# Optimization experiments

Measured on AMD Instinct MI355X. Metric: run time of the kernel, lower is better.

Reference implementation:

```python
import jax, jax.numpy as jnp
import numpy as np

N_NODES = 100000
N_EDGES = 1600000
NODE_DIM = 64
EDGE_DIM = 16
HIDDEN = 64
N_LAYERS = 3
N_GRAPHS = 512
BN_EPS = 1e-5


def setup_inputs() -> dict:
    key = jax.random.key(0)
    ks = jax.random.split(key, 12)
    x = jax.random.normal(ks[0], (N_NODES, NODE_DIM), dtype=jnp.float32)
    edge_index = jax.random.randint(ks[1], (2, N_EDGES), 0, N_NODES, dtype=jnp.int32)
    edge_attr = jax.random.normal(ks[2], (N_EDGES, EDGE_DIM), dtype=jnp.float32)
    batch = jnp.sort(jax.random.randint(ks[3], (N_NODES,), 0, N_GRAPHS, dtype=jnp.int32))
    s = 0.1
    # stacked per-layer params (node_dim == hidden so all layers share shapes)
    We = jax.random.normal(ks[4], (N_LAYERS, EDGE_DIM, HIDDEN), dtype=jnp.float32) * s
    be = jnp.zeros((N_LAYERS, HIDDEN), dtype=jnp.float32)
    W1 = jax.random.normal(ks[5], (N_LAYERS, HIDDEN, HIDDEN), dtype=jnp.float32) * s
    b1 = jnp.zeros((N_LAYERS, HIDDEN), dtype=jnp.float32)
    W2 = jax.random.normal(ks[6], (N_LAYERS, HIDDEN, HIDDEN), dtype=jnp.float32) * s
    b2 = jnp.zeros((N_LAYERS, HIDDEN), dtype=jnp.float32)
    gamma = jnp.ones((N_LAYERS, HIDDEN), dtype=jnp.float32)
    beta = jnp.zeros((N_LAYERS, HIDDEN), dtype=jnp.float32)
    return {"x": x, "edge_attr": edge_attr, "We": We, "be": be, "W1": W1,
            "b1": b1, "W2": W2, "b2": b2, "gamma": gamma, "beta": beta,
            "edge_index": edge_index, "batch": batch}


def reference(x, edge_attr, We, be, W1, b1, W2, b2, gamma, beta, edge_index, batch):
    src, dst = edge_index[0], edge_index[1]
    n_nodes = x.shape[0]
    z = x
    zs = []
    for l in range(We.shape[0]):
        # GINEConv: message = relu(x_j + Lin(edge_attr)); aggr = scatter_add at dst
        e = edge_attr @ We[l] + be[l]                       # [E, H]
        msg = jax.nn.relu(z[src] + e)                       # [E, H]
        aggr = jax.ops.segment_sum(msg, dst, num_segments=n_nodes)  # [N, H]
        h = z + aggr                                        # (1 + eps)*x, eps=0
        h = jax.nn.relu(h @ W1[l] + b1[l]) @ W2[l] + b2[l]  # GINE nn MLP
        h = jax.nn.relu(h)
        # BatchNorm1d in training mode: biased batch stats over nodes
        mean = jnp.mean(h, axis=0)
        var = jnp.mean(jnp.square(h - mean), axis=0)
        h = gamma[l] * (h - mean) * jax.lax.rsqrt(var + BN_EPS) + beta[l]
        z = h
        zs.append(h)
    zz = jnp.concatenate(zs, axis=1)                        # [N, L*H]
    g = jax.ops.segment_sum(zz, batch, num_segments=N_GRAPHS)  # [G, L*H]
    return zz, g
```

## Files before the change

kernel.cpp:

```cpp
#include <hip/hip_runtime.h>

#define N_NODES 100000
#define N_EDGES 1600000
#define HIDDEN 64
#define EDGE_DIM 16
#define N_LAYERS 3
#define N_GRAPHS 512
#define BN_EPS 1e-5f

#define CHUNK 2048
#define NCHUNK ((N_NODES + CHUNK - 1) / CHUNK)

typedef _Float16 h2 __attribute__((ext_vector_type(2)));
typedef _Float16 h4 __attribute__((ext_vector_type(4)));


__global__ void k_hist(const int* __restrict__ dst, int* __restrict__ hist) {
    int e = blockIdx.x * 256 + threadIdx.x;
    if (e < N_EDGES) atomicAdd(&hist[dst[e]], 1);
}

__global__ void k_scan_partial(const int* __restrict__ hist, int* __restrict__ partial) {
    __shared__ int sd[256];
    int c = blockIdx.x, t = threadIdx.x;
    int base = c * CHUNK + t * 8;
    int s = 0;
#pragma unroll
    for (int u = 0; u < 8; ++u) {
        int i = base + u;
        s += (i < N_NODES) ? hist[i] : 0;
    }
    sd[t] = s;
    __syncthreads();
    for (int d = 128; d > 0; d >>= 1) {
        if (t < d) sd[t] += sd[t + d];
        __syncthreads();
    }
    if (t == 0) partial[c] = sd[0];
}

__global__ void k_scan_base(const int* __restrict__ partial, int* __restrict__ cbase) {
    if (threadIdx.x == 0) {
        int r = 0;
        for (int c = 0; c < NCHUNK; ++c) { cbase[c] = r; r += partial[c]; }
    }
}

__global__ void k_scan_final(const int* __restrict__ hist, const int* __restrict__ cbase,
                             int* __restrict__ row_start, int* __restrict__ cursor) {
    __shared__ int sd[256];
    int c = blockIdx.x, t = threadIdx.x;
    int i0 = c * CHUNK + t * 8;
    int v[8];
    int s = 0;
#pragma unroll
    for (int u = 0; u < 8; ++u) {
        int i = i0 + u;
        v[u] = (i < N_NODES) ? hist[i] : 0;
        s += v[u];
    }
    sd[t] = s;
    __syncthreads();
    for (int d = 1; d < 256; d <<= 1) {
        int x = (t >= d) ? sd[t - d] : 0;
        __syncthreads();
        sd[t] += x;
        __syncthreads();
    }
    int run = cbase[c] + sd[t] - s;
#pragma unroll
    for (int u = 0; u < 8; ++u) {
        int i = i0 + u;
        if (i <= N_NODES) { row_start[i] = run; cursor[i] = run; }
        run += v[u];
    }
}

__global__ void k_fill_es(const int* __restrict__ edge_index, int* __restrict__ cursor,
                          int2* __restrict__ es_sorted) {
    int e = blockIdx.x * 256 + threadIdx.x;
    if (e >= N_EDGES) return;
    int s = edge_index[e];
    int d = edge_index[N_EDGES + e];
    int p = atomicAdd(&cursor[d], 1);
    es_sorted[p] = make_int2(e, s);
}

__global__ __launch_bounds__(256) void k_gather(const int2* __restrict__ es,
        const float* __restrict__ ea, _Float16* __restrict__ ea16,
        int* __restrict__ src_sorted) {
    int gid = blockIdx.x * 256 + threadIdx.x;
    if (gid >= N_EDGES * 4) return;
    int p = gid >> 2, part = gid & 3;
    int2 r = es[p];
    if (part == 0) src_sorted[p] = r.y;
    float4 v = ((const float4*)(ea + (size_t)r.x * 16))[part];
    h4 o = {(_Float16)v.x, (_Float16)v.y, (_Float16)v.z, (_Float16)v.w};
    ((h4*)(ea16 + (size_t)p * 16))[part] = o;
}

__global__ __launch_bounds__(256) void k_cvt_x(const float* __restrict__ x,
                                               _Float16* __restrict__ x16) {
    int i = blockIdx.x * 256 + threadIdx.x;
    if (i >= N_NODES * 16) return;
    float4 v = ((const float4*)x)[i];
    h4 o = {(_Float16)v.x, (_Float16)v.y, (_Float16)v.z, (_Float16)v.w};
    ((h4*)x16)[i] = o;
}


__global__ __launch_bounds__(256) void k_aggregate(
        const float* __restrict__ zself_base, int zstride,
        const _Float16* __restrict__ z16,
        const float* __restrict__ We, const float* __restrict__ be,
        const int* __restrict__ row_start,
        const int* __restrict__ srcs, const _Float16* __restrict__ ea16,
        float* __restrict__ hin) {
    int gid = blockIdx.x * 256 + threadIdx.x;
    int node = __builtin_amdgcn_readfirstlane(gid >> 6);
    int lane = threadIdx.x & 63;
    if (node >= N_NODES) return;
    h2 w2[8];
#pragma unroll
    for (int i = 0; i < 8; ++i) {
        h2 t;
        t[0] = (_Float16)We[(2 * i) * 64 + lane];
        t[1] = (_Float16)We[(2 * i + 1) * 64 + lane];
        w2[i] = t;
    }
    float bl = be[lane];
    int p0 = row_start[node], p1 = row_start[node + 1];
    float acc = 0.f;
    int p = p0;
    for (; p + 8 <= p1; p += 8) {
        int s[8];
        float zv[8], ev[8];
#pragma unroll
        for (int u = 0; u < 8; ++u) s[u] = srcs[p + u];
#pragma unroll
        for (int u = 0; u < 8; ++u) zv[u] = (float)z16[(size_t)s[u] * 64 + lane];
#pragma unroll
        for (int u = 0; u < 8; ++u) {
            const h2* row = (const h2*)(ea16 + (size_t)(p + u) * 16);
            float e = bl;
#pragma unroll
            for (int i = 0; i < 8; ++i) e = __builtin_amdgcn_fdot2(row[i], w2[i], e, false);
            ev[u] = e;
        }
#pragma unroll
        for (int u = 0; u < 8; ++u) acc += fmaxf(zv[u] + ev[u], 0.f);
    }
    for (; p + 4 <= p1; p += 4) {
        int s[4];
        float zv[4], ev[4];
#pragma unroll
        for (int u = 0; u < 4; ++u) s[u] = srcs[p + u];
#pragma unroll
        for (int u = 0; u < 4; ++u) zv[u] = (float)z16[(size_t)s[u] * 64 + lane];
#pragma unroll
        for (int u = 0; u < 4; ++u) {
            const h2* row = (const h2*)(ea16 + (size_t)(p + u) * 16);
            float e = bl;
#pragma unroll
            for (int i = 0; i < 8; ++i) e = __builtin_amdgcn_fdot2(row[i], w2[i], e, false);
            ev[u] = e;
        }
#pragma unroll
        for (int u = 0; u < 4; ++u) acc += fmaxf(zv[u] + ev[u], 0.f);
    }
    for (; p < p1; ++p) {
        int s = srcs[p];
        const h2* row = (const h2*)(ea16 + (size_t)p * 16);
        float zv = (float)z16[(size_t)s * 64 + lane];
        float e = bl;
#pragma unroll
        for (int i = 0; i < 8; ++i) e = __builtin_amdgcn_fdot2(row[i], w2[i], e, false);
        acc += fmaxf(zv + e, 0.f);
    }
    float zself = zself_base[(size_t)node * zstride + lane];
    hin[(size_t)node * 64 + lane] = zself + acc;
}

__global__ __launch_bounds__(256) void k_mlp(
        const float* __restrict__ hin,
        const float* __restrict__ W1, const float* __restrict__ b1,
        const float* __restrict__ W2, const float* __restrict__ b2,
        float* __restrict__ hout) {
    int n = blockIdx.x * 256 + threadIdx.x;
    if (n >= N_NODES) return;
    const float4* __restrict__ hv = (const float4*)(hin + (size_t)n * 64);
    float t[64];
#pragma unroll
    for (int j = 0; j < 64; ++j) t[j] = b1[j];
    for (int kc = 0; kc < 16; ++kc) {
        float4 h4v = hv[kc];
        const float* wr = W1 + kc * 4 * 64;
#pragma unroll
        for (int j = 0; j < 64; ++j) t[j] = fmaf(h4v.x, wr[j], t[j]);
#pragma unroll
        for (int j = 0; j < 64; ++j) t[j] = fmaf(h4v.y, wr[64 + j], t[j]);
#pragma unroll
        for (int j = 0; j < 64; ++j) t[j] = fmaf(h4v.z, wr[128 + j], t[j]);
#pragma unroll
        for (int j = 0; j < 64; ++j) t[j] = fmaf(h4v.w, wr[192 + j], t[j]);
    }
#pragma unroll
    for (int j = 0; j < 64; ++j) t[j] = fmaxf(t[j], 0.f);
    float o[64];
#pragma unroll
    for (int j = 0; j < 64; ++j) o[j] = b2[j];
#pragma unroll
    for (int k = 0; k < 64; ++k) {
        const float* wr = W2 + k * 64;
        float tk = t[k];
#pragma unroll
        for (int j = 0; j < 64; ++j) o[j] = fmaf(tk, wr[j], o[j]);
    }
    float4* ov = (float4*)(hout + (size_t)n * 64);
#pragma unroll
    for (int i = 0; i < 16; ++i) {
        float4 v;
        v.x = fmaxf(o[4 * i + 0], 0.f);
        v.y = fmaxf(o[4 * i + 1], 0.f);
        v.z = fmaxf(o[4 * i + 2], 0.f);
        v.w = fmaxf(o[4 * i + 3], 0.f);
        ov[i] = v;
    }
}

__global__ __launch_bounds__(256) void k_stats(const float* __restrict__ h,
                                               float* __restrict__ ssum, float* __restrict__ ssq) {
    __shared__ float ls[64], lq[64];
    int tid = blockIdx.x * 256 + threadIdx.x;
    int nth = gridDim.x * 256;
    float4 s = {0, 0, 0, 0}, q = {0, 0, 0, 0};
    const float4* hv = (const float4*)h;
    for (int i = tid; i < N_NODES * 16; i += nth) {
        float4 v = hv[i];
        s.x += v.x; s.y += v.y; s.z += v.z; s.w += v.w;
        q.x += v.x * v.x; q.y += v.y * v.y; q.z += v.z * v.z; q.w += v.w * v.w;
    }
    if (threadIdx.x < 64) { ls[threadIdx.x] = 0.f; lq[threadIdx.x] = 0.f; }
    __syncthreads();
    int j = (threadIdx.x & 15) * 4;
    atomicAdd(&ls[j + 0], s.x); atomicAdd(&ls[j + 1], s.y);
    atomicAdd(&ls[j + 2], s.z); atomicAdd(&ls[j + 3], s.w);
    atomicAdd(&lq[j + 0], q.x); atomicAdd(&lq[j + 1], q.y);
    atomicAdd(&lq[j + 2], q.z); atomicAdd(&lq[j + 3], q.w);
    __syncthreads();
    if (threadIdx.x < 64) {
        atomicAdd(&ssum[threadIdx.x], ls[threadIdx.x]);
        atomicAdd(&ssq[threadIdx.x], lq[threadIdx.x]);
    }
}

__global__ __launch_bounds__(256) void k_norm(const float* __restrict__ h,
        const float* __restrict__ ssum, const float* __restrict__ ssq,
        const float* __restrict__ gamma, const float* __restrict__ beta,
        float* __restrict__ zzslice, _Float16* __restrict__ z16out) {
    int i = blockIdx.x * 256 + threadIdx.x;
    if (i >= N_NODES * 16) return;
    int n = i >> 4, j4 = i & 15;
    int j = j4 * 4;
    float4 v = ((const float4*)h)[i];
    float out[4];
#pragma unroll
    for (int u = 0; u < 4; ++u) {
        float mean = ssum[j + u] * (1.f / N_NODES);
        float var = ssq[j + u] * (1.f / N_NODES) - mean * mean;
        float scale = gamma[j + u] * rsqrtf(var + BN_EPS);
        float shift = beta[j + u] - mean * scale;
        float hv = (u == 0) ? v.x : (u == 1) ? v.y : (u == 2) ? v.z : v.w;
        out[u] = fmaf(hv, scale, shift);
    }
    float4 r = {out[0], out[1], out[2], out[3]};
    *(float4*)(zzslice + (size_t)n * 192 + j4 * 4) = r;
    if (z16out) {
        h4 o = {(_Float16)out[0], (_Float16)out[1], (_Float16)out[2], (_Float16)out[3]};
        ((h4*)(z16out + (size_t)n * 64 + j))[0] = o;
    }
}

#define GNODES 64
__global__ __launch_bounds__(192) void k_graph(const float* __restrict__ zz,
                                               const int* __restrict__ batch, float* __restrict__ g) {
    int j = threadIdx.x;
    int n0 = blockIdx.x * GNODES;
    int n1 = n0 + GNODES;
    if (n1 > N_NODES) n1 = N_NODES;
    if (n0 >= N_NODES) return;
    float acc = 0.f;
    int cur = batch[n0];
    for (int n = n0; n < n1; ++n) {
        int b = batch[n];
        if (b != cur) {
            atomicAdd(&g[(size_t)cur * 192 + j], acc);
            acc = 0.f;
            cur = b;
        }
        acc += zz[(size_t)n * 192 + j];
    }
    atomicAdd(&g[(size_t)cur * 192 + j], acc);
}


extern "C" void kernel_launch(void* const* d_in, const int* in_sizes, int n_in,
                              void* d_out, int out_size, void* d_ws, size_t ws_size,
                              hipStream_t stream) {
    const float* x         = (const float*)d_in[0];
    const float* edge_attr = (const float*)d_in[1];
    const float* We        = (const float*)d_in[2];
    const float* be        = (const float*)d_in[3];
    const float* W1        = (const float*)d_in[4];
    const float* b1        = (const float*)d_in[5];
    const float* W2        = (const float*)d_in[6];
    const float* b2        = (const float*)d_in[7];
    const float* gamma     = (const float*)d_in[8];
    const float* beta      = (const float*)d_in[9];
    const int* edge_index  = (const int*)d_in[10];
    const int* batch       = (const int*)d_in[11];

    float* zz = (float*)d_out;
    float* g  = zz + (size_t)N_NODES * 192;

    char* ws = (char*)d_ws;
    size_t off = 0;
    auto alloc = [&](size_t bytes) {
        void* p = ws + off;
        off = (off + bytes + 255) & ~(size_t)255;
        return p;
    };
    int* hist        = (int*)alloc((size_t)N_NODES * 4);
    int* row_start   = (int*)alloc((size_t)(N_NODES + 1) * 4);
    int* cursor      = (int*)alloc((size_t)(N_NODES + 1) * 4);
    int* partial     = (int*)alloc(64 * 4);
    int* cbase       = (int*)alloc(64 * 4);
    int2* es_sorted  = (int2*)alloc((size_t)N_EDGES * 8);
    int* src_sorted  = (int*)alloc((size_t)N_EDGES * 4);
    _Float16* ea16   = (_Float16*)alloc((size_t)N_EDGES * 16 * 2);
    _Float16* x16    = (_Float16*)alloc((size_t)N_NODES * 64 * 2);
    _Float16* z16    = (_Float16*)alloc((size_t)N_NODES * 64 * 2);
    float* hin       = (float*)alloc((size_t)N_NODES * 64 * 4);
    float* hout      = (float*)alloc((size_t)N_NODES * 64 * 4);
    float* ssum      = (float*)alloc((size_t)N_LAYERS * 64 * 4);
    float* ssq       = (float*)alloc((size_t)N_LAYERS * 64 * 4);

    hipMemsetAsync(hist, 0, (size_t)N_NODES * 4, stream);
    k_hist<<<(N_EDGES + 255) / 256, 256, 0, stream>>>(edge_index + N_EDGES, hist);
    k_scan_partial<<<NCHUNK, 256, 0, stream>>>(hist, partial);
    k_scan_base<<<1, 64, 0, stream>>>(partial, cbase);
    k_scan_final<<<NCHUNK, 256, 0, stream>>>(hist, cbase, row_start, cursor);
    k_fill_es<<<(N_EDGES + 255) / 256, 256, 0, stream>>>(edge_index, cursor, es_sorted);
    k_gather<<<(N_EDGES * 4 + 255) / 256, 256, 0, stream>>>(
        es_sorted, edge_attr, ea16, src_sorted);
    k_cvt_x<<<(N_NODES * 16 + 255) / 256, 256, 0, stream>>>(x, x16);

    hipMemsetAsync(g, 0, (size_t)N_GRAPHS * 192 * 4, stream);
    hipMemsetAsync(ssum, 0, (size_t)N_LAYERS * 64 * 4, stream);
    hipMemsetAsync(ssq, 0, (size_t)N_LAYERS * 64 * 4, stream);

    for (int l = 0; l < N_LAYERS; ++l) {
        const float* zself = (l == 0) ? x : (zz + (size_t)(l - 1) * 64);
        int zstride = (l == 0) ? 64 : 192;
        const _Float16* zsrc16 = (l == 0) ? x16 : z16;
        k_aggregate<<<(N_NODES * 64 + 255) / 256, 256, 0, stream>>>(
            zself, zstride, zsrc16,
            We + (size_t)l * EDGE_DIM * 64, be + (size_t)l * 64,
            row_start, src_sorted, ea16, hin);
        k_mlp<<<(N_NODES + 255) / 256, 256, 0, stream>>>(
            hin, W1 + (size_t)l * 4096, b1 + (size_t)l * 64,
            W2 + (size_t)l * 4096, b2 + (size_t)l * 64, hout);
        k_stats<<<256, 256, 0, stream>>>(hout, ssum + l * 64, ssq + l * 64);
        k_norm<<<(N_NODES * 16 + 255) / 256, 256, 0, stream>>>(
            hout, ssum + l * 64, ssq + l * 64,
            gamma + (size_t)l * 64, beta + (size_t)l * 64,
            zz + (size_t)l * 64, (l < N_LAYERS - 1) ? z16 : (_Float16*)nullptr);
    }
    k_graph<<<(N_NODES + GNODES - 1) / GNODES, 192, 0, stream>>>(zz, batch, g);
}
```

Baseline: 997.4 us.

## Replace per-node atomic CSR fill with two-level bucketed counting sort

Edges are now sorted by destination in two stages. First they are scattered into 3125 buckets of 32 destination nodes each, which cuts contention on the global atomic cursors. A per-bucket kernel then ranks edges within the bucket using shared-memory atomics and writes src_sorted and the fp16 edge attributes directly, which removes the separate es_sorted gather pass. The aggregate kernel also loads each fp16 edge row as two 16-byte vectors and drops the 4-wide remainder loop. The new path adds launches (k_bcount, k_bscan, k_bscatter) and packs the low destination bits into the edge id, which caps edge ids at 2^27.

```diff
diff --git a/kernel.cpp b/kernel.cpp
--- a/kernel.cpp
+++ b/kernel.cpp
@@ -11,6 +11,10 @@
 #define CHUNK 2048
 #define NCHUNK ((N_NODES + CHUNK - 1) / CHUNK)
 
+#define BSHIFT 5
+#define NBUCK (N_NODES >> BSHIFT)
+#define EMASK 0x07FFFFFF
+
 typedef _Float16 h2 __attribute__((ext_vector_type(2)));
 typedef _Float16 h4 __attribute__((ext_vector_type(4)));
 
@@ -47,7 +51,7 @@
 }
 
 __global__ void k_scan_final(const int* __restrict__ hist, const int* __restrict__ cbase,
-                             int* __restrict__ row_start, int* __restrict__ cursor) {
+                             int* __restrict__ row_start) {
     __shared__ int sd[256];
     int c = blockIdx.x, t = threadIdx.x;
     int i0 = c * CHUNK + t * 8;
@@ -71,32 +75,96 @@
 #pragma unroll
     for (int u = 0; u < 8; ++u) {
         int i = i0 + u;
-        if (i <= N_NODES) { row_start[i] = run; cursor[i] = run; }
+        if (i <= N_NODES) row_start[i] = run;
         run += v[u];
     }
 }
 
-__global__ void k_fill_es(const int* __restrict__ edge_index, int* __restrict__ cursor,
-                          int2* __restrict__ es_sorted) {
+
+__global__ __launch_bounds__(256) void k_bcount(const int* __restrict__ dst,
+                                                int* __restrict__ bcount) {
+    __shared__ int lh[NBUCK];
+    for (int i = threadIdx.x; i < NBUCK; i += 256) lh[i] = 0;
+    __syncthreads();
+    int tid = blockIdx.x * 256 + threadIdx.x;
+    for (int e = tid; e < N_EDGES; e += gridDim.x * 256)
+        atomicAdd(&lh[dst[e] >> BSHIFT], 1);
+    __syncthreads();
+    for (int i = threadIdx.x; i < NBUCK; i += 256) {
+        int v = lh[i];
+        if (v) atomicAdd(&bcount[i], v);
+    }
+}
+
+__global__ __launch_bounds__(256) void k_bscan(const int* __restrict__ bcount,
+                                               int* __restrict__ bstart, int* __restrict__ bcur) {
+    __shared__ int sd[256];
+    const int PER = (NBUCK + 255) / 256;
+    int t = threadIdx.x;
+    int base = t * PER;
+    int s = 0;
+#pragma unroll
+    for (int u = 0; u < PER; ++u) {
+        int i = base + u;
+        if (i < NBUCK) s += bcount[i];
+    }
+    sd[t] = s;
+    __syncthreads();
+    for (int d = 1; d < 256; d <<= 1) {
+        int x = (t >= d) ? sd[t - d] : 0;
+        __syncthreads();
+        sd[t] += x;
+        __syncthreads();
+    }
+    int run = sd[t] - s;
+#pragma unroll
+    for (int u = 0; u < PER; ++u) {
+        int i = base + u;
+        if (i < NBUCK) {
+            bstart[i] = run;
+            bcur[i] = run;
+            run += bcount[i];
+        }
+    }
+    if (t == 255) bstart[NBUCK] = N_EDGES;
+}
+
+__global__ void k_bscatter(const int* __restrict__ edge_index, int* __restrict__ bcur,
+                           int2* __restrict__ brec) {
     int e = blockIdx.x * 256 + threadIdx.x;
     if (e >= N_EDGES) return;
     int s = edge_index[e];
     int d = edge_index[N_EDGES + e];
-    int p = atomicAdd(&cursor[d], 1);
-    es_sorted[p] = make_int2(e, s);
-}
-
-__global__ __launch_bounds__(256) void k_gather(const int2* __restrict__ es,
+    int pos = atomicAdd(&bcur[d >> BSHIFT], 1);
+    brec[pos] = make_int2(e | ((d & 31) << 27), s);
+}
+
+__global__ __launch_bounds__(256) void k_bfinal(const int2* __restrict__ brec,
+        const int* __restrict__ bstart, const int* __restrict__ row_start,
         const float* __restrict__ ea, _Float16* __restrict__ ea16,
         int* __restrict__ src_sorted) {
-    int gid = blockIdx.x * 256 + threadIdx.x;
-    if (gid >= N_EDGES * 4) return;
-    int p = gid >> 2, part = gid & 3;
-    int2 r = es[p];
-    if (part == 0) src_sorted[p] = r.y;
-    float4 v = ((const float4*)(ea + (size_t)r.x * 16))[part];
-    h4 o = {(_Float16)v.x, (_Float16)v.y, (_Float16)v.z, (_Float16)v.w};
-    ((h4*)(ea16 + (size_t)p * 16))[part] = o;
+    __shared__ int cnt[32];
+    int b = blockIdx.x;
+    if (threadIdx.x < 32) cnt[threadIdx.x] = 0;
+    __syncthreads();
+    int r0 = bstart[b], r1 = bstart[b + 1];
+    for (int i = r0 + threadIdx.x; i < r1; i += 256) {
+        int2 rec = brec[i];
+        int e = rec.x & EMASK;
+        int lo5 = (unsigned)rec.x >> 27;
+        int dst = (b << BSHIFT) | lo5;
+        int rank = atomicAdd(&cnt[lo5], 1);
+        int p = row_start[dst] + rank;
+        const float4* er = (const float4*)(ea + (size_t)e * 16);
+        float4 v0 = er[0], v1 = er[1], v2 = er[2], v3 = er[3];
+        h4* op = (h4*)(ea16 + (size_t)p * 16);
+        h4 o0 = {(_Float16)v0.x, (_Float16)v0.y, (_Float16)v0.z, (_Float16)v0.w};
+        h4 o1 = {(_Float16)v1.x, (_Float16)v1.y, (_Float16)v1.z, (_Float16)v1.w};
+        h4 o2 = {(_Float16)v2.x, (_Float16)v2.y, (_Float16)v2.z, (_Float16)v2.w};
+        h4 o3 = {(_Float16)v3.x, (_Float16)v3.y, (_Float16)v3.z, (_Float16)v3.w};
+        op[0] = o0; op[1] = o1; op[2] = o2; op[3] = o3;
+        src_sorted[p] = rec.y;
+    }
 }
 
 __global__ __launch_bounds__(256) void k_cvt_x(const float* __restrict__ x,
@@ -141,40 +209,36 @@
         for (int u = 0; u < 8; ++u) zv[u] = (float)z16[(size_t)s[u] * 64 + lane];
 #pragma unroll
         for (int u = 0; u < 8; ++u) {
-            const h2* row = (const h2*)(ea16 + (size_t)(p + u) * 16);
+            const uint4* rv = (const uint4*)(ea16 + (size_t)(p + u) * 16);
+            uint4 a = rv[0], bq = rv[1];
             float e = bl;
-#pragma unroll
-            for (int i = 0; i < 8; ++i) e = __builtin_amdgcn_fdot2(row[i], w2[i], e, false);
+            e = __builtin_amdgcn_fdot2(__builtin_bit_cast(h2, a.x), w2[0], e, false);
+            e = __builtin_amdgcn_fdot2(__builtin_bit_cast(h2, a.y), w2[1], e, false);
+            e = __builtin_amdgcn_fdot2(__builtin_bit_cast(h2, a.z), w2[2], e, false);
+            e = __builtin_amdgcn_fdot2(__builtin_bit_cast(h2, a.w), w2[3], e, false);
+            e = __builtin_amdgcn_fdot2(__builtin_bit_cast(h2, bq.x), w2[4], e, false);
+            e = __builtin_amdgcn_fdot2(__builtin_bit_cast(h2, bq.y), w2[5], e, false);
+            e = __builtin_amdgcn_fdot2(__builtin_bit_cast(h2, bq.z), w2[6], e, false);
+            e = __builtin_amdgcn_fdot2(__builtin_bit_cast(h2, bq.w), w2[7], e, false);
             ev[u] = e;
         }
 #pragma unroll
         for (int u = 0; u < 8; ++u) acc += fmaxf(zv[u] + ev[u], 0.f);
     }
-    for (; p + 4 <= p1; p += 4) {
-        int s[4];
-        float zv[4], ev[4];
-#pragma unroll
-        for (int u = 0; u < 4; ++u) s[u] = srcs[p + u];
-#pragma unroll
-        for (int u = 0; u < 4; ++u) zv[u] = (float)z16[(size_t)s[u] * 64 + lane];
-#pragma unroll
-        for (int u = 0; u < 4; ++u) {
-            const h2* row = (const h2*)(ea16 + (size_t)(p + u) * 16);
-            float e = bl;
-#pragma unroll
-            for (int i = 0; i < 8; ++i) e = __builtin_amdgcn_fdot2(row[i], w2[i], e, false);
-            ev[u] = e;
-        }
-#pragma unroll
-        for (int u = 0; u < 4; ++u) acc += fmaxf(zv[u] + ev[u], 0.f);
-    }
     for (; p < p1; ++p) {
         int s = srcs[p];
-        const h2* row = (const h2*)(ea16 + (size_t)p * 16);
         float zv = (float)z16[(size_t)s * 64 + lane];
+        const uint4* rv = (const uint4*)(ea16 + (size_t)p * 16);
+        uint4 a = rv[0], bq = rv[1];
         float e = bl;
-#pragma unroll
-        for (int i = 0; i < 8; ++i) e = __builtin_amdgcn_fdot2(row[i], w2[i], e, false);
+        e = __builtin_amdgcn_fdot2(__builtin_bit_cast(h2, a.x), w2[0], e, false);
+        e = __builtin_amdgcn_fdot2(__builtin_bit_cast(h2, a.y), w2[1], e, false);
+        e = __builtin_amdgcn_fdot2(__builtin_bit_cast(h2, a.z), w2[2], e, false);
+        e = __builtin_amdgcn_fdot2(__builtin_bit_cast(h2, a.w), w2[3], e, false);
+        e = __builtin_amdgcn_fdot2(__builtin_bit_cast(h2, bq.x), w2[4], e, false);
+        e = __builtin_amdgcn_fdot2(__builtin_bit_cast(h2, bq.y), w2[5], e, false);
+        e = __builtin_amdgcn_fdot2(__builtin_bit_cast(h2, bq.z), w2[6], e, false);
+        e = __builtin_amdgcn_fdot2(__builtin_bit_cast(h2, bq.w), w2[7], e, false);
         acc += fmaxf(zv + e, 0.f);
     }
     float zself = zself_base[(size_t)node * zstride + lane];
@@ -332,10 +396,12 @@
     };
     int* hist        = (int*)alloc((size_t)N_NODES * 4);
     int* row_start   = (int*)alloc((size_t)(N_NODES + 1) * 4);
-    int* cursor      = (int*)alloc((size_t)(N_NODES + 1) * 4);
     int* partial     = (int*)alloc(64 * 4);
     int* cbase       = (int*)alloc(64 * 4);
-    int2* es_sorted  = (int2*)alloc((size_t)N_EDGES * 8);
+    int* bcount      = (int*)alloc((size_t)NBUCK * 4);
+    int* bstart      = (int*)alloc((size_t)(NBUCK + 1) * 4);
+    int* bcur        = (int*)alloc((size_t)NBUCK * 4);
+    int2* brec       = (int2*)alloc((size_t)N_EDGES * 8);
     int* src_sorted  = (int*)alloc((size_t)N_EDGES * 4);
     _Float16* ea16   = (_Float16*)alloc((size_t)N_EDGES * 16 * 2);
     _Float16* x16    = (_Float16*)alloc((size_t)N_NODES * 64 * 2);
@@ -346,13 +412,16 @@
     float* ssq       = (float*)alloc((size_t)N_LAYERS * 64 * 4);
 
     hipMemsetAsync(hist, 0, (size_t)N_NODES * 4, stream);
+    hipMemsetAsync(bcount, 0, (size_t)NBUCK * 4, stream);
     k_hist<<<(N_EDGES + 255) / 256, 256, 0, stream>>>(edge_index + N_EDGES, hist);
     k_scan_partial<<<NCHUNK, 256, 0, stream>>>(hist, partial);
     k_scan_base<<<1, 64, 0, stream>>>(partial, cbase);
-    k_scan_final<<<NCHUNK, 256, 0, stream>>>(hist, cbase, row_start, cursor);
-    k_fill_es<<<(N_EDGES + 255) / 256, 256, 0, stream>>>(edge_index, cursor, es_sorted);
-    k_gather<<<(N_EDGES * 4 + 255) / 256, 256, 0, stream>>>(
-        es_sorted, edge_attr, ea16, src_sorted);
+    k_scan_final<<<NCHUNK, 256, 0, stream>>>(hist, cbase, row_start);
+
+    k_bcount<<<256, 256, 0, stream>>>(edge_index + N_EDGES, bcount);
+    k_bscan<<<1, 256, 0, stream>>>(bcount, bstart, bcur);
+    k_bscatter<<<(N_EDGES + 255) / 256, 256, 0, stream>>>(edge_index, bcur, brec);
+    k_bfinal<<<NBUCK, 256, 0, stream>>>(brec, bstart, row_start, edge_attr, ea16, src_sorted);
     k_cvt_x<<<(N_NODES * 16 + 255) / 256, 256, 0, stream>>>(x, x16);
 
     hipMemsetAsync(g, 0, (size_t)N_GRAPHS * 192 * 4, stream);
```

Result: slower. 1.061 ms (+6.4%).
